# Performance work log

Hardware: AMD Instinct MI355X
Metric: run time of the kernel (lower is better)

The kernel has to match this reference:

```python
import jax, jax.numpy as jnp
import numpy as np

N = 100000   # nodes
E = 1600000  # edges
R = 8        # relations
B = 8        # bases (min(R, hidden))
IN = 128; HID = 128; OUT = 128
BN_EPS = 1e-5


def setup_inputs() -> dict:
    key = jax.random.key(0)
    ks = jax.random.split(key, 20)
    s = 0.1  # xavier-ish small gain as in reset_parameters
    f32 = jnp.float32
    inp = {
        'x': jax.random.normal(ks[0], (N, IN), f32),
        'edge_index': jax.random.randint(ks[1], (2, E), 0, N, dtype=jnp.int32),
        'edge_type': jax.random.randint(ks[2], (E,), 0, R, dtype=jnp.int32),
        # RGCNConv layer 1 (basis decomposition)
        'basis1': jax.random.normal(ks[3], (B, IN, HID), f32) * s,
        'comp1': jax.random.normal(ks[4], (R, B), f32) * s,
        'root1': jax.random.normal(ks[5], (IN, HID), f32) * s,
        'bias1': jnp.zeros((HID,), f32),
        # layer 2
        'basis2': jax.random.normal(ks[6], (B, HID, HID), f32) * s,
        'comp2': jax.random.normal(ks[7], (R, B), f32) * s,
        'root2': jax.random.normal(ks[8], (HID, HID), f32) * s,
        'bias2': jnp.zeros((HID,), f32),
        # layer 3
        'basis3': jax.random.normal(ks[9], (B, HID, OUT), f32) * s,
        'comp3': jax.random.normal(ks[10], (R, B), f32) * s,
        'root3': jax.random.normal(ks[11], (HID, OUT), f32) * s,
        'bias3': jnp.zeros((OUT,), f32),
        # BatchNorm affine params (batch-stat normalization)
        'bn1_gamma': jnp.ones((HID,), f32),
        'bn1_beta': jnp.zeros((HID,), f32),
        'bn2_gamma': jnp.ones((HID,), f32),
        'bn2_beta': jnp.zeros((HID,), f32),
    }
    return inp


def rgcn_conv(x, basis, comp, root, bias, src, dst, etype):
    # relation weights from basis decomposition: W[r] = sum_b comp[r,b] * basis[b]
    W = jnp.einsum('rb,bio->rio', comp, basis)  # [R, in, out]
    # mean aggregation per (dst, relation); transform after mean (linearity)
    seg = dst.astype(jnp.int32) * R + etype.astype(jnp.int32)  # [E]
    msg_sum = jax.ops.segment_sum(x[src], seg, num_segments=N * R)  # [N*R, in]
    cnt = jax.ops.segment_sum(jnp.ones((src.shape[0],), x.dtype), seg, num_segments=N * R)
    mean = msg_sum / jnp.maximum(cnt, 1.0)[:, None]
    mean = mean.reshape(N, R, -1)  # [N, R, in]
    out = jnp.einsum('nri,rio->no', mean, W) + x @ root + bias
    return out


def batchnorm(h, gamma, beta):
    m = h.mean(axis=0)
    v = h.var(axis=0)
    return (h - m) * jax.lax.rsqrt(v + BN_EPS) * gamma + beta


def reference(x, edge_index, edge_type,
              basis1, comp1, root1, bias1,
              basis2, comp2, root2, bias2,
              basis3, comp3, root3, bias3,
              bn1_gamma, bn1_beta, bn2_gamma, bn2_beta):
    src, dst = edge_index[0], edge_index[1]
    h = rgcn_conv(x, basis1, comp1, root1, bias1, src, dst, edge_type)
    h = batchnorm(h, bn1_gamma, bn1_beta)
    h = jnp.where(h > 0, h, 0.1 * h)  # LeakyReLU(0.1); dropout inactive (eval)
    h = rgcn_conv(h, basis2, comp2, root2, bias2, src, dst, edge_type)
    h = batchnorm(h, bn2_gamma, bn2_beta)
    h = jnp.where(h > 0, h, 0.1 * h)
    h = rgcn_conv(h, basis3, comp3, root3, bias3, src, dst, edge_type)
    # F.normalize(p=2, dim=1)
    norm = jnp.maximum(jnp.sqrt(jnp.sum(h * h, axis=1, keepdims=True)), 1e-12)
    return h / norm
```

## Files before the change

### kernel.cpp

```cpp
#include <hip/hip_runtime.h>

#define NN 100000
#define EE 1600000
#define RRR 8
#define NSEG (NN*RRR)
#define F 128
#define KDIM 1152
#define NKT 36
#define BNEPS 1e-5f

typedef __attribute__((ext_vector_type(8))) short bf16x8;
typedef __attribute__((ext_vector_type(8))) unsigned short u16x8;
typedef __attribute__((ext_vector_type(4))) float f32x4;

static __device__ __forceinline__ unsigned short bf16r(float f) {
  unsigned u = __float_as_uint(f);
  u += 0x7fffu + ((u >> 16) & 1u);
  return (unsigned short)(u >> 16);
}
static __device__ __forceinline__ float b2f(unsigned short s) {
  return __uint_as_float((unsigned)s << 16);
}

__global__ __launch_bounds__(256) void k_precnt(const float* __restrict__ x,
    unsigned short* __restrict__ xb, const int* __restrict__ dst,
    const int* __restrict__ et, unsigned* __restrict__ cnt) {
  int idx = blockIdx.x*256 + threadIdx.x;
  if (idx < NN*32) {
    float4 v = ((const float4*)x)[idx];
    ushort4 o;
    o.x = bf16r(v.x); o.y = bf16r(v.y); o.z = bf16r(v.z); o.w = bf16r(v.w);
    ((ushort4*)xb)[idx] = o;
  }
  if (idx < EE)
    atomicAdd(&cnt[dst[idx]*RRR + et[idx]], 1u);
}

__global__ void k_scan1(const unsigned* __restrict__ cnt, unsigned* __restrict__ off,
                        unsigned* __restrict__ bsum) {
  __shared__ unsigned s[256];
  int t = threadIdx.x;
  int base = blockIdx.x*2048 + t*8;
  unsigned loc[8];
  unsigned tot = 0;
#pragma unroll
  for (int j = 0; j < 8; j++) {
    unsigned v = (base+j < NSEG) ? cnt[base+j] : 0u;
    loc[j] = tot;
    tot += v;
  }
  s[t] = tot;
  __syncthreads();
  for (int d = 1; d < 256; d <<= 1) {
    unsigned v = (t >= d) ? s[t-d] : 0u;
    __syncthreads();
    s[t] += v;
    __syncthreads();
  }
  unsigned tbase = s[t] - tot;
#pragma unroll
  for (int j = 0; j < 8; j++)
    if (base+j < NSEG) off[base+j] = tbase + loc[j];
  if (t == 255) bsum[blockIdx.x] = s[255];
}

__global__ void k_scan2(unsigned* bsum, int nb) {
  __shared__ unsigned s[512];
  int t = threadIdx.x;
  unsigned v = (t < nb) ? bsum[t] : 0u;
  s[t] = v;
  __syncthreads();
  for (int d = 1; d < 512; d <<= 1) {
    unsigned u = (t >= d) ? s[t-d] : 0u;
    __syncthreads();
    s[t] += u;
    __syncthreads();
  }
  if (t < nb) bsum[t] = (t == 0) ? 0u : s[t-1];
}

__global__ void k_scan3(unsigned* off, const unsigned* __restrict__ bsum) {
  int i = blockIdx.x*256 + threadIdx.x;
  if (i < NSEG) off[i] += bsum[i >> 11];
}

__global__ void k_fill(const int* __restrict__ src, const int* __restrict__ dst,
                       const int* __restrict__ et, unsigned* __restrict__ off,
                       int* __restrict__ csr) {
  int e = blockIdx.x*256 + threadIdx.x;
  if (e < EE) {
    int seg = dst[e]*RRR + et[e];
    unsigned pos = atomicAdd(&off[seg], 1u);
    csr[pos] = src[e];
  }
}

__global__ void k_makeW3(const float* __restrict__ b1, const float* __restrict__ c1,
                         const float* __restrict__ r1, const float* __restrict__ b2,
                         const float* __restrict__ c2, const float* __restrict__ r2,
                         const float* __restrict__ b3, const float* __restrict__ c3,
                         const float* __restrict__ r3, unsigned short* __restrict__ WB3,
                         float* __restrict__ stats) {
  int kt = blockIdx.x, ct = blockIdx.y, l = blockIdx.z;
  int lane = threadIdx.x;
  if (kt == 0 && ct == 0 && l == 0) {
#pragma unroll
    for (int j = 0; j < 8; j++) stats[lane*8 + j] = 0.f;
  }
  const float* basis = (l == 0) ? b1 : (l == 1) ? b2 : b3;
  const float* comp  = (l == 0) ? c1 : (l == 1) ? c2 : c3;
  const float* root  = (l == 0) ? r1 : (l == 1) ? r2 : r3;
  int o = ct*16 + (lane & 15);
  int kbase = kt*32 + (lane >> 4)*8;
  unsigned short v[8];
#pragma unroll
  for (int j = 0; j < 8; j++) {
    int k = kbase + j;
    float val;
    if (k < 1024) {
      int r = k >> 7, i = k & 127;
      val = 0.f;
#pragma unroll
      for (int bb = 0; bb < 8; bb++)
        val += comp[r*8+bb] * basis[(bb*F + i)*F + o];
    } else {
      val = root[(k - 1024)*F + o];
    }
    v[j] = bf16r(val);
  }
  unsigned short* dstp = WB3 + (size_t)l*KDIM*F + ((size_t)(kt*8 + ct)*64 + lane)*8;
#pragma unroll
  for (int j = 0; j < 8; j++) dstp[j] = v[j];
}

__global__ __launch_bounds__(256) void k_agg(const unsigned short* __restrict__ hb,
    const unsigned* __restrict__ off, const unsigned* __restrict__ cnt,
    const int* __restrict__ csr, unsigned short* __restrict__ Mean, int segBase) {
  int t = threadIdx.x;
  int sl = t & 15, c8 = sl*8;
  int g = t >> 4;
  int s0 = segBase + blockIdx.x*32 + 2*g;
  int s1 = s0 + 1;
  unsigned cA = cnt[s0], cB = cnt[s1];
  unsigned bA = off[s0] - cA, bB = off[s1] - cB;
  const unsigned short* hc = hb + c8;
  float aA[8], aB[8];
#pragma unroll
  for (int u = 0; u < 8; u++) { aA[u] = 0.f; aB[u] = 0.f; }
  unsigned jA = 0, jB = 0;
  while (jA < cA || jB < cB) {
    unsigned nA = cA - jA; if (nA > 2) nA = 2;
    unsigned nB = cB - jB; if (nB > 2) nB = 2;
    int i0 = 0, i1 = 0, i2 = 0, i3 = 0;
    if (nA > 0) i0 = csr[bA + jA];
    if (nA > 1) i1 = csr[bA + jA + 1];
    if (nB > 0) i2 = csr[bB + jB];
    if (nB > 1) i3 = csr[bB + jB + 1];
    if (nA > 0) {
      u16x8 v = *(const u16x8*)&hc[(size_t)i0*F];
#pragma unroll
      for (int u = 0; u < 8; u++) aA[u] += b2f(v[u]);
    }
    if (nA > 1) {
      u16x8 v = *(const u16x8*)&hc[(size_t)i1*F];
#pragma unroll
      for (int u = 0; u < 8; u++) aA[u] += b2f(v[u]);
    }
    if (nB > 0) {
      u16x8 v = *(const u16x8*)&hc[(size_t)i2*F];
#pragma unroll
      for (int u = 0; u < 8; u++) aB[u] += b2f(v[u]);
    }
    if (nB > 1) {
      u16x8 v = *(const u16x8*)&hc[(size_t)i3*F];
#pragma unroll
      for (int u = 0; u < 8; u++) aB[u] += b2f(v[u]);
    }
    jA += nA; jB += nB;
  }
  float ivA = cA ? 1.f/(float)cA : 0.f;
  float ivB = cB ? 1.f/(float)cB : 0.f;
  u16x8 oA, oB;
#pragma unroll
  for (int u = 0; u < 8; u++) { oA[u] = bf16r(aA[u]*ivA); oB[u] = bf16r(aB[u]*ivB); }
  int l0 = s0 - segBase, l1 = s1 - segBase;
  *(u16x8*)&Mean[(size_t)(l0 >> 3)*KDIM + (l0 & 7)*F + c8] = oA;
  *(u16x8*)&Mean[(size_t)(l1 >> 3)*KDIM + (l1 & 7)*F + c8] = oB;
  if ((s0 & 7) == 0) {
    int node = s0 >> 3;
    *(u16x8*)&Mean[(size_t)(l0 >> 3)*KDIM + 1024 + c8] =
        *(const u16x8*)&hb[(size_t)node*F + c8];
  }
}

__global__ __launch_bounds__(256) void k_gemm(const unsigned short* __restrict__ Mean,
    const unsigned short* __restrict__ WB, const float* __restrict__ bias,
    float* __restrict__ outp, float* __restrict__ stats,
    int outBase, int count, int mode) {
  __shared__ float s_sum[128];
  __shared__ float s_sq[128];
  int t = threadIdx.x;
  int wave = t >> 6;
  int lane = t & 63;
  int rbase = blockIdx.x*128 + wave*32;
  int rlo = lane & 15;
  int kg = lane >> 4;
  int r0 = rbase + rlo;       if (r0 > count-1) r0 = count-1;
  int r1 = rbase + 16 + rlo;  if (r1 > count-1) r1 = count-1;
  const unsigned short* a0p = Mean + (size_t)r0*KDIM + kg*8;
  const unsigned short* a1p = Mean + (size_t)r1*KDIM + kg*8;
  const unsigned short* bp  = WB + (size_t)lane*8;

  if (mode == 0 && t < 128) { s_sum[t] = 0.f; s_sq[t] = 0.f; }

  f32x4 acc[2][8];
#pragma unroll
  for (int i = 0; i < 2; i++)
#pragma unroll
    for (int j = 0; j < 8; j++) acc[i][j] = (f32x4){0.f,0.f,0.f,0.f};

  for (int kt = 0; kt < NKT; kt++) {
    bf16x8 a0 = *(const bf16x8*)(a0p + kt*32);
    bf16x8 a1 = *(const bf16x8*)(a1p + kt*32);
#pragma unroll
    for (int ct = 0; ct < 8; ct++) {
      bf16x8 b = *(const bf16x8*)(bp + (size_t)(kt*8 + ct)*64*8);
      acc[0][ct] = __builtin_amdgcn_mfma_f32_16x16x32_bf16(a0, b, acc[0][ct], 0, 0, 0);
      acc[1][ct] = __builtin_amdgcn_mfma_f32_16x16x32_bf16(a1, b, acc[1][ct], 0, 0, 0);
    }
  }

  float bv[8];
#pragma unroll
  for (int ct = 0; ct < 8; ct++) bv[ct] = bias[ct*16 + rlo];

  if (mode == 0) {
    __syncthreads();
    float psum[8], psq[8];
#pragma unroll
    for (int ct = 0; ct < 8; ct++) { psum[ct] = 0.f; psq[ct] = 0.f; }
#pragma unroll
    for (int rt = 0; rt < 2; rt++) {
#pragma unroll
      for (int i = 0; i < 4; i++) {
        int row = rbase + rt*16 + kg*4 + i;
        if (row < count) {
          float* orow = outp + (size_t)(outBase + row)*F;
#pragma unroll
          for (int ct = 0; ct < 8; ct++) {
            float y = acc[rt][ct][i] + bv[ct];
            orow[ct*16 + rlo] = y;
            psum[ct] += y;
            psq[ct]  += y*y;
          }
        }
      }
    }
#pragma unroll
    for (int ct = 0; ct < 8; ct++) {
      atomicAdd(&s_sum[ct*16 + rlo], psum[ct]);
      atomicAdd(&s_sq [ct*16 + rlo], psq[ct]);
    }
    __syncthreads();
    if (t < 128) {
      atomicAdd(&stats[t],       s_sum[t]);
      atomicAdd(&stats[128 + t], s_sq[t]);
    }
  } else {
#pragma unroll
    for (int rt = 0; rt < 2; rt++) {
#pragma unroll
      for (int i = 0; i < 4; i++) {
        int row = rbase + rt*16 + kg*4 + i;
        float y[8], ss = 0.f;
#pragma unroll
        for (int ct = 0; ct < 8; ct++) {
          y[ct] = acc[rt][ct][i] + bv[ct];
          ss += y[ct]*y[ct];
        }
#pragma unroll
        for (int m = 1; m < 16; m <<= 1)
          ss += __shfl_xor(ss, m, 64);
        float inv = 1.f / fmaxf(sqrtf(ss), 1e-12f);
        if (row < count) {
          float* orow = outp + (size_t)(outBase + row)*F;
#pragma unroll
          for (int ct = 0; ct < 8; ct++)
            orow[ct*16 + rlo] = y[ct]*inv;
        }
      }
    }
  }
}

__global__ __launch_bounds__(256) void k_bnapply(const float* __restrict__ h,
    const float* __restrict__ stats, const float* __restrict__ gamma,
    const float* __restrict__ beta, unsigned short* __restrict__ outp) {
  int idx = blockIdx.x*256 + threadIdx.x;
  if (idx >= NN*32) return;
  int row = idx >> 5;
  int c4 = (idx & 31) * 4;
  float4 v  = *(const float4*)&h[(size_t)row*F + c4];
  float4 sm = *(const float4*)&stats[c4];
  float4 sq = *(const float4*)&stats[128 + c4];
  float4 gm = *(const float4*)&gamma[c4];
  float4 bt = *(const float4*)&beta[c4];
  const float invN = 1.f / (float)NN;
  ushort4 o;
  { float m = sm.x*invN; float var = sq.x*invN - m*m; float r0 = rsqrtf(var + BNEPS);
    float z = (v.x - m)*r0*gm.x + bt.x; o.x = bf16r((z > 0.f) ? z : 0.1f*z); }
  { float m = sm.y*invN; float var = sq.y*invN - m*m; float r0 = rsqrtf(var + BNEPS);
    float z = (v.y - m)*r0*gm.y + bt.y; o.y = bf16r((z > 0.f) ? z : 0.1f*z); }
  { float m = sm.z*invN; float var = sq.z*invN - m*m; float r0 = rsqrtf(var + BNEPS);
    float z = (v.z - m)*r0*gm.z + bt.z; o.z = bf16r((z > 0.f) ? z : 0.1f*z); }
  { float m = sm.w*invN; float var = sq.w*invN - m*m; float r0 = rsqrtf(var + BNEPS);
    float z = (v.w - m)*r0*gm.w + bt.w; o.w = bf16r((z > 0.f) ? z : 0.1f*z); }
  *(ushort4*)&outp[(size_t)row*F + c4] = o;
}

extern "C" void kernel_launch(void* const* d_in, const int* in_sizes, int n_in,
                              void* d_out, int out_size, void* d_ws, size_t ws_size,
                              hipStream_t stream) {
  const float* x      = (const float*)d_in[0];
  const int*   ei     = (const int*)d_in[1];
  const int*   etp    = (const int*)d_in[2];
  const float* basis[3] = {(const float*)d_in[3], (const float*)d_in[7],  (const float*)d_in[11]};
  const float* comp[3]  = {(const float*)d_in[4], (const float*)d_in[8],  (const float*)d_in[12]};
  const float* root[3]  = {(const float*)d_in[5], (const float*)d_in[9],  (const float*)d_in[13]};
  const float* bias[3]  = {(const float*)d_in[6], (const float*)d_in[10], (const float*)d_in[14]};
  const float* gamma[2] = {(const float*)d_in[15], (const float*)d_in[17]};
  const float* beta[2]  = {(const float*)d_in[16], (const float*)d_in[18]};
  const int* srcv = ei;
  const int* dstv = ei + EE;
  float* out = (float*)d_out;

  char* w = (char*)d_ws;
  size_t p = 0;
  auto take = [&](size_t bytes) -> void* {
    void* q = w + p;
    p = (p + bytes + 255) & ~(size_t)255;
    return q;
  };
  unsigned* cnt   = (unsigned*)take((size_t)NSEG*4);
  unsigned* off   = (unsigned*)take((size_t)NSEG*4);
  int*      csr   = (int*)     take((size_t)EE*4);
  unsigned* bsum  = (unsigned*)take(1024*4);
  unsigned short* WB3 = (unsigned short*)take((size_t)3*KDIM*F*2);
  float*    stats = (float*)   take(512*4);
  float*    wsA   = (float*)   take((size_t)NN*F*4);
  unsigned short* wsBb = (unsigned short*)take((size_t)NN*F*2);
  unsigned short* xb   = (unsigned short*)take((size_t)NN*F*2);
  size_t avail = (ws_size > p) ? (ws_size - p) : 0;
  long long chmax = (long long)(avail / ((size_t)KDIM*2));
  int CH = (chmax > NN) ? NN : (int)(chmax & ~3LL);
  if (CH < 4) CH = 4;
  unsigned short* Mean = (unsigned short*)(w + p);

  hipMemsetAsync(cnt, 0, (size_t)NSEG*4, stream);
  k_precnt<<<12500, 256, 0, stream>>>(x, xb, dstv, etp, cnt);
  int nb1 = (NSEG + 2047)/2048;
  k_scan1<<<nb1, 256, 0, stream>>>(cnt, off, bsum);
  k_scan2<<<1, 512, 0, stream>>>(bsum, nb1);
  k_scan3<<<(NSEG+255)/256, 256, 0, stream>>>(off, bsum);
  k_fill<<<(EE+255)/256, 256, 0, stream>>>(srcv, dstv, etp, off, csr);
  dim3 gw(NKT, 8, 3);
  k_makeW3<<<gw, 64, 0, stream>>>(basis[0], comp[0], root[0],
                                  basis[1], comp[1], root[1],
                                  basis[2], comp[2], root[2], WB3, stats);

  for (int l = 0; l < 3; l++) {
    const unsigned short* hin = (l == 0) ? xb : wsBb;
    float* hraw = (l == 2) ? out : wsA;
    int mode = (l == 2) ? 1 : 0;
    const unsigned short* WB = WB3 + (size_t)l*KDIM*F;
    float* st = stats + (size_t)(l == 2 ? 0 : l)*256;
    for (int b0n = 0; b0n < NN; b0n += CH) {
      int cc = NN - b0n; if (cc > CH) cc = CH;
      k_agg<<<cc/4, 256, 0, stream>>>(hin, off, cnt, csr, Mean, b0n*8);
      k_gemm<<<(cc+127)/128, 256, 0, stream>>>(Mean, WB, bias[l], hraw, st, b0n, cc, mode);
    }
    if (l < 2)
      k_bnapply<<<12500, 256, 0, stream>>>(hraw, stats + (size_t)l*256, gamma[l], beta[l], wsBb);
  }
}
```

Baseline: 1.066 ms.

## Store aggregated means in MFMA-fragment-tiled layout and use one row tile per wave

The aggregation kernel now writes the mean/root-concatenated A matrix in a pre-swizzled layout where each 16-row by 32-k tile is contiguous in lane order. The GEMM then reads A with fully coalesced 16-byte-per-lane loads instead of strided row reads. Each wave now computes a single 16-row tile rather than two, doubling the number of GEMM blocks but halving per-wave B reuse, and the chunk size is rounded to multiples of 64. Tail tiles past count read unwritten buffer memory, but those rows are masked on store.

```diff
diff --git a/kernel.cpp b/kernel.cpp
--- a/kernel.cpp
+++ b/kernel.cpp
@@ -184,12 +184,20 @@
 #pragma unroll
   for (int u = 0; u < 8; u++) { oA[u] = bf16r(aA[u]*ivA); oB[u] = bf16r(aB[u]*ivB); }
   int l0 = s0 - segBase, l1 = s1 - segBase;
-  *(u16x8*)&Mean[(size_t)(l0 >> 3)*KDIM + (l0 & 7)*F + c8] = oA;
-  *(u16x8*)&Mean[(size_t)(l1 >> 3)*KDIM + (l1 & 7)*F + c8] = oB;
-  if ((s0 & 7) == 0) {
-    int node = s0 >> 3;
-    *(u16x8*)&Mean[(size_t)(l0 >> 3)*KDIM + 1024 + c8] =
-        *(const u16x8*)&hb[(size_t)node*F + c8];
+  int ktl = sl >> 2, kgl = sl & 3;
+  {
+    int nl = l0 >> 3, r = l0 & 7;
+    size_t ci = ((size_t)((nl >> 4)*NKT + r*4 + ktl)*64 + (nl & 15) + 16*kgl);
+    *(u16x8*)&Mean[ci*8] = oA;
+    if (r == 0) {
+      size_t cs = ((size_t)((nl >> 4)*NKT + 32 + ktl)*64 + (nl & 15) + 16*kgl);
+      *(u16x8*)&Mean[cs*8] = *(const u16x8*)&hb[(size_t)(s0 >> 3)*F + c8];
+    }
+  }
+  {
+    int nl = l1 >> 3, r = l1 & 7;
+    size_t ci = ((size_t)((nl >> 4)*NKT + r*4 + ktl)*64 + (nl & 15) + 16*kgl);
+    *(u16x8*)&Mean[ci*8] = oB;
   }
 }
 
@@ -202,31 +210,25 @@
   int t = threadIdx.x;
   int wave = t >> 6;
   int lane = t & 63;
-  int rbase = blockIdx.x*128 + wave*32;
+  int rt = blockIdx.x*4 + wave;
+  int rbase = rt*16;
   int rlo = lane & 15;
   int kg = lane >> 4;
-  int r0 = rbase + rlo;       if (r0 > count-1) r0 = count-1;
-  int r1 = rbase + 16 + rlo;  if (r1 > count-1) r1 = count-1;
-  const unsigned short* a0p = Mean + (size_t)r0*KDIM + kg*8;
-  const unsigned short* a1p = Mean + (size_t)r1*KDIM + kg*8;
-  const unsigned short* bp  = WB + (size_t)lane*8;
+  const unsigned short* ap = Mean + ((size_t)rt*NKT*64 + lane)*8;
+  const unsigned short* bp = WB + (size_t)lane*8;
 
   if (mode == 0 && t < 128) { s_sum[t] = 0.f; s_sq[t] = 0.f; }
 
-  f32x4 acc[2][8];
-#pragma unroll
-  for (int i = 0; i < 2; i++)
-#pragma unroll
-    for (int j = 0; j < 8; j++) acc[i][j] = (f32x4){0.f,0.f,0.f,0.f};
+  f32x4 acc[8];
+#pragma unroll
+  for (int j = 0; j < 8; j++) acc[j] = (f32x4){0.f,0.f,0.f,0.f};
 
   for (int kt = 0; kt < NKT; kt++) {
-    bf16x8 a0 = *(const bf16x8*)(a0p + kt*32);
-    bf16x8 a1 = *(const bf16x8*)(a1p + kt*32);
+    bf16x8 a = *(const bf16x8*)(ap + (size_t)kt*512);
 #pragma unroll
     for (int ct = 0; ct < 8; ct++) {
-      bf16x8 b = *(const bf16x8*)(bp + (size_t)(kt*8 + ct)*64*8);
-      acc[0][ct] = __builtin_amdgcn_mfma_f32_16x16x32_bf16(a0, b, acc[0][ct], 0, 0, 0);
-      acc[1][ct] = __builtin_amdgcn_mfma_f32_16x16x32_bf16(a1, b, acc[1][ct], 0, 0, 0);
+      bf16x8 b = *(const bf16x8*)(bp + (size_t)(kt*8 + ct)*512);
+      acc[ct] = __builtin_amdgcn_mfma_f32_16x16x32_bf16(a, b, acc[ct], 0, 0, 0);
     }
   }
 
@@ -240,19 +242,16 @@
 #pragma unroll
     for (int ct = 0; ct < 8; ct++) { psum[ct] = 0.f; psq[ct] = 0.f; }
 #pragma unroll
-    for (int rt = 0; rt < 2; rt++) {
-#pragma unroll
-      for (int i = 0; i < 4; i++) {
-        int row = rbase + rt*16 + kg*4 + i;
-        if (row < count) {
-          float* orow = outp + (size_t)(outBase + row)*F;
-#pragma unroll
-          for (int ct = 0; ct < 8; ct++) {
-            float y = acc[rt][ct][i] + bv[ct];
-            orow[ct*16 + rlo] = y;
-            psum[ct] += y;
-            psq[ct]  += y*y;
-          }
+    for (int i = 0; i < 4; i++) {
+      int row = rbase + kg*4 + i;
+      if (row < count) {
+        float* orow = outp + (size_t)(outBase + row)*F;
+#pragma unroll
+        for (int ct = 0; ct < 8; ct++) {
+          float y = acc[ct][i] + bv[ct];
+          orow[ct*16 + rlo] = y;
+          psum[ct] += y;
+          psq[ct]  += y*y;
         }
       }
     }
@@ -268,26 +267,23 @@
     }
   } else {
 #pragma unroll
-    for (int rt = 0; rt < 2; rt++) {
-#pragma unroll
-      for (int i = 0; i < 4; i++) {
-        int row = rbase + rt*16 + kg*4 + i;
-        float y[8], ss = 0.f;
-#pragma unroll
-        for (int ct = 0; ct < 8; ct++) {
-          y[ct] = acc[rt][ct][i] + bv[ct];
-          ss += y[ct]*y[ct];
-        }
-#pragma unroll
-        for (int m = 1; m < 16; m <<= 1)
-          ss += __shfl_xor(ss, m, 64);
-        float inv = 1.f / fmaxf(sqrtf(ss), 1e-12f);
-        if (row < count) {
-          float* orow = outp + (size_t)(outBase + row)*F;
-#pragma unroll
-          for (int ct = 0; ct < 8; ct++)
-            orow[ct*16 + rlo] = y[ct]*inv;
-        }
+    for (int i = 0; i < 4; i++) {
+      int row = rbase + kg*4 + i;
+      float y[8], ss = 0.f;
+#pragma unroll
+      for (int ct = 0; ct < 8; ct++) {
+        y[ct] = acc[ct][i] + bv[ct];
+        ss += y[ct]*y[ct];
+      }
+#pragma unroll
+      for (int m = 1; m < 16; m <<= 1)
+        ss += __shfl_xor(ss, m, 64);
+      float inv = 1.f / fmaxf(sqrtf(ss), 1e-12f);
+      if (row < count) {
+        float* orow = outp + (size_t)(outBase + row)*F;
+#pragma unroll
+        for (int ct = 0; ct < 8; ct++)
+          orow[ct*16 + rlo] = y[ct]*inv;
       }
     }
   }
@@ -352,8 +348,8 @@
   unsigned short* xb   = (unsigned short*)take((size_t)NN*F*2);
   size_t avail = (ws_size > p) ? (ws_size - p) : 0;
   long long chmax = (long long)(avail / ((size_t)KDIM*2));
-  int CH = (chmax > NN) ? NN : (int)(chmax & ~3LL);
-  if (CH < 4) CH = 4;
+  int CH = (chmax > NN) ? NN : (int)(chmax & ~63LL);
+  if (CH < 64) CH = 64;
   unsigned short* Mean = (unsigned short*)(w + p);
 
   hipMemsetAsync(cnt, 0, (size_t)NSEG*4, stream);
@@ -377,7 +373,7 @@
     for (int b0n = 0; b0n < NN; b0n += CH) {
       int cc = NN - b0n; if (cc > CH) cc = CH;
       k_agg<<<cc/4, 256, 0, stream>>>(hin, off, cnt, csr, Mean, b0n*8);
-      k_gemm<<<(cc+127)/128, 256, 0, stream>>>(Mean, WB, bias[l], hraw, st, b0n, cc, mode);
+      k_gemm<<<(cc+63)/64, 256, 0, stream>>>(Mean, WB, bias[l], hraw, st, b0n, cc, mode);
     }
     if (l < 2)
       k_bnapply<<<12500, 256, 0, stream>>>(hraw, stats + (size_t)l*256, gamma[l], beta[l], wsBb);
```

Result: slower. 1.166 ms (+9.4%).
